# Kernel optimization log

Hardware: AMD Instinct MI355X
Metric: run time of the kernel (lower is better)

## Reference

```python
import jax, jax.numpy as jnp
import numpy as np

N, M, E = 50000, 10000, 600000
IN, H, OUT = 128, 128, 64
SLOPE = 0.01      # nn.LeakyReLU default
ATT_SLOPE = 0.2   # GAT-style attention slope
EPS = 1e-5


def _act(v):
    return jax.nn.leaky_relu(v, SLOPE)


def _graph_norm(x, w, b, a):
    # PyG GraphNorm over the node/hyperedge dim (single graph)
    mu = jnp.mean(x, axis=0, keepdims=True)
    xc = x - a * mu
    var = jnp.mean(xc * xc, axis=0, keepdims=True)
    return w * xc * jax.lax.rsqrt(var + EPS) + b


def setup_inputs() -> dict:
    key = jax.random.key(0)
    ks = iter(jax.random.split(key, 40))
    def nrm(shape):
        return jax.random.normal(next(ks), shape, jnp.float32)
    def wgt(shape):
        return nrm(shape) / np.float32(np.sqrt(shape[0]))
    return dict(
        x=nrm((N, IN)), x_struct=nrm((N, IN)), x_e=nrm((M, IN)),
        node_idx=jax.random.randint(next(ks), (E,), 0, N, dtype=jnp.int32),
        hedge_idx=jax.random.randint(next(ks), (E,), 0, M, dtype=jnp.int32),
        her_W1=wgt((IN, H)), her_b1=jnp.zeros((H,), jnp.float32),
        her_W2=wgt((H, H)), her_b2=jnp.zeros((H,), jnp.float32),
        sr_W1=wgt((IN, H)), sr_b1=jnp.zeros((H,), jnp.float32),
        sr_W2=wgt((H, H)), sr_b2=jnp.zeros((H,), jnp.float32),
        att_Wq=wgt((H, H)), att_Wk=wgt((H, H)), att_Wv=wgt((H, H)),
        ef_W=wgt((2 * H, H)), ef_b=jnp.zeros((H,), jnp.float32),
        gn1_w=jnp.ones((2 * H,), jnp.float32), gn1_b=jnp.zeros((2 * H,), jnp.float32), gn1_a=jnp.ones((2 * H,), jnp.float32),
        gn2_w=jnp.ones((H,), jnp.float32), gn2_b=jnp.zeros((H,), jnp.float32), gn2_a=jnp.ones((H,), jnp.float32),
        cls_W1=wgt((H, H)), cls_b1=jnp.zeros((H,), jnp.float32),
        cls_W2=wgt((H, OUT)), cls_b2=jnp.zeros((OUT,), jnp.float32),
    )


def _forward(x, x_struct, x_e,
             her_W1, her_b1, her_W2, her_b2,
             sr_W1, sr_b1, sr_W2, sr_b2,
             att_Wq, att_Wk, att_Wv,
             ef_W, ef_b,
             gn1_w, gn1_b, gn1_a, gn2_w, gn2_b, gn2_a,
             cls_W1, cls_b1, cls_W2, cls_b2,
             node_idx, hedge_idx):
    # --- SemanticHyperedgeRefiner: MLP [M, IN] -> [M, H]
    xe = _act(x_e @ her_W1 + her_b1) @ her_W2 + her_b2

    # --- SemanticFeatureRefiner: MLP + one node->hyperedge->node mean MP round
    h = _act(x @ sr_W1 + sr_b1)                                               # [N, H]
    ones = jnp.ones((E,), h.dtype)
    cnt_e_raw = jax.ops.segment_sum(ones, hedge_idx, M)                        # edges per hyperedge
    cnt_v_raw = jax.ops.segment_sum(ones, node_idx, N)                         # edges per node
    cnt_e = jnp.maximum(cnt_e_raw, 1.0)
    cnt_v = jnp.maximum(cnt_v_raw, 1.0)
    m_e = jax.ops.segment_sum(h[node_idx], hedge_idx, M) / cnt_e[:, None]      # [M, H]
    m_v = jax.ops.segment_sum(m_e[hedge_idx], node_idx, N) / cnt_v[:, None]    # [N, H]
    h = _act((h + m_v) @ sr_W2 + sr_b2)                                        # [N, H]

    # --- NodeHyperedgeAttention: GAT-style segment softmax per node over incident hyperedges
    q, k, v = h @ att_Wq, xe @ att_Wk, xe @ att_Wv
    s = jax.nn.leaky_relu(jnp.sum(q[node_idx] * k[hedge_idx], axis=1) / np.float32(np.sqrt(H)), ATT_SLOPE)  # [E]
    smax = jax.ops.segment_max(s, node_idx, N)
    e = jnp.exp(s - smax[node_idx])
    denom = jnp.maximum(jax.ops.segment_sum(e, node_idx, N), 1e-16)
    alpha = e / denom[node_idx]
    h = jax.ops.segment_sum(alpha[:, None] * v[hedge_idx], node_idx, N)        # [N, H]

    # --- MinAggregation: scatter-min node features into hyperedges
    agg = jax.ops.segment_min(h[node_idx], hedge_idx, M)                       # [M, H]
    agg = jnp.where((cnt_e_raw > 0.5)[:, None], agg, 0.0)                      # zero empty segments

    # --- edge_fusion: GraphNorm -> Linear(2H,H) -> LeakyReLU -> GraphNorm, then outer activation
    z = jnp.concatenate([agg, xe], axis=1)                                     # [M, 2H]
    z = _graph_norm(z, gn1_w, gn1_b, gn1_a)
    z = _act(z @ ef_W + ef_b)
    z = _graph_norm(z, gn2_w, gn2_b, gn2_a)
    z = _act(z)

    # --- Classifier (dropout inactive in eval)
    z = _act(z @ cls_W1 + cls_b1)
    return z @ cls_W2 + cls_b2                                                 # [M, OUT]


def reference(x, x_struct, x_e, node_idx, hedge_idx,
              her_W1, her_b1, her_W2, her_b2,
              sr_W1, sr_b1, sr_W2, sr_b2,
              att_Wq, att_Wk, att_Wv,
              ef_W, ef_b,
              gn1_w, gn1_b, gn1_a, gn2_w, gn2_b, gn2_a,
              cls_W1, cls_b1, cls_W2, cls_b2):
    return _forward(x, x_struct, x_e,
                    her_W1, her_b1, her_W2, her_b2,
                    sr_W1, sr_b1, sr_W2, sr_b2,
                    att_Wq, att_Wk, att_Wv,
                    ef_W, ef_b,
                    gn1_w, gn1_b, gn1_a, gn2_w, gn2_b, gn2_a,
                    cls_W1, cls_b1, cls_W2, cls_b2,
                    node_idx, hedge_idx)
```

## Files before the change

### kernel.cpp

```cpp
#include <hip/hip_runtime.h>
#include <float.h>
#include <math.h>

#define HF 128
#define SCAN_CHUNK 4096
#define NB_CSR 128
#define VPACK 12500
#define VRANGE (2 * VPACK)
#define CS_GRID 256

static inline int idiv(int a, int b) { return (a + b - 1) / b; }

__device__ inline unsigned short f2bf(float x) {
  unsigned u = __float_as_uint(x);
  return (unsigned short)((u + 0x7fffu + ((u >> 16) & 1u)) >> 16);
}
__device__ inline unsigned packbf(float a, float b) {
  return (unsigned)f2bf(a) | ((unsigned)f2bf(b) << 16);
}
#define BFLO(w) __uint_as_float((w) << 16)
#define BFHI(w) __uint_as_float((w) & 0xffff0000u)


__global__ __launch_bounds__(512) void csr_hist(const int* __restrict__ nidx,
                                                const int* __restrict__ hidx,
                                                int E, int M,
                                                int* __restrict__ HE,
                                                int* __restrict__ HV) {
  __shared__ int bins[VPACK];
  int b = blockIdx.x, y = blockIdx.y, tid = threadIdx.x;
  int chunk = (E + NB_CSR - 1) / NB_CSR;
  int e0 = b * chunk;
  int e1 = e0 + chunk; if (e1 > E) e1 = E;
  if (y == 0) {
    for (int s = tid; s < M; s += 512) bins[s] = 0;
    __syncthreads();
    for (int e = e0 + tid; e < e1; e += 512) atomicAdd(&bins[hidx[e]], 1);
    __syncthreads();
    for (int s = tid; s < M; s += 512) HE[(size_t)b * M + s] = bins[s];
  } else {
    int R = (y - 1) * VRANGE;
    int* HVr = HV + ((size_t)(y - 1) * NB_CSR + b) * VPACK;
    for (int q = tid; q < VPACK; q += 512) bins[q] = 0;
    __syncthreads();
    for (int e = e0 + tid; e < e1; e += 512) {
      int v = nidx[e] - R;
      if ((unsigned)v < (unsigned)VRANGE) atomicAdd(&bins[v >> 1], (v & 1) ? 0x10000 : 1);
    }
    __syncthreads();
    for (int q = tid; q < VPACK; q += 512) HVr[q] = bins[q];
  }
}

__global__ __launch_bounds__(256) void csr_colscan(int* __restrict__ HE,
                                                   int* __restrict__ HV,
                                                   int M, int N, int NVR,
                                                   int* __restrict__ cnt_e,
                                                   int* __restrict__ cnt_v) {
  int col = blockIdx.x * 256 + threadIdx.x;
  if (col < M) {
    int run = 0;
    for (int b = 0; b < NB_CSR; ++b) {
      size_t i = (size_t)b * M + col;
      int t = HE[i]; HE[i] = run; run += t;
    }
    cnt_e[col] = run;
  } else if (col < M + NVR * VPACK) {
    int c = col - M;
    int r = c / VPACK, q = c - r * VPACK;
    int* HVr = HV + (size_t)r * NB_CSR * VPACK;
    int run = 0;
    for (int b = 0; b < NB_CSR; ++b) {
      size_t i = (size_t)b * VPACK + q;
      int t = HVr[i]; HVr[i] = run; run += t;
    }
    int node = r * VRANGE + 2 * q;
    if (node < N) cnt_v[node] = run & 0xffff;
    if (node + 1 < N) cnt_v[node + 1] = run >> 16;
  }
}

__global__ __launch_bounds__(512) void csr_scatter(const int* __restrict__ nidx,
                                                   const int* __restrict__ hidx,
                                                   int E, int M,
                                                   const int* __restrict__ HE,
                                                   const int* __restrict__ HV,
                                                   const int* __restrict__ off_e,
                                                   const int* __restrict__ off_v,
                                                   unsigned short* __restrict__ by_h,
                                                   unsigned short* __restrict__ by_v) {
  __shared__ int bins[VPACK];
  int b = blockIdx.x, y = blockIdx.y, tid = threadIdx.x;
  int chunk = (E + NB_CSR - 1) / NB_CSR;
  int e0 = b * chunk;
  int e1 = e0 + chunk; if (e1 > E) e1 = E;
  if (y == 0) {
    for (int s = tid; s < M; s += 512) bins[s] = off_e[s] + HE[(size_t)b * M + s];
    __syncthreads();
    for (int e = e0 + tid; e < e1; e += 512) {
      int pos = atomicAdd(&bins[hidx[e]], 1);
      by_h[pos] = (unsigned short)nidx[e];
    }
  } else {
    int R = (y - 1) * VRANGE;
    const int* HVr = HV + ((size_t)(y - 1) * NB_CSR + b) * VPACK;
    for (int q = tid; q < VPACK; q += 512) bins[q] = HVr[q];
    __syncthreads();
    for (int e = e0 + tid; e < e1; e += 512) {
      int v = nidx[e];
      int vr = v - R;
      if ((unsigned)vr < (unsigned)VRANGE) {
        int old = atomicAdd(&bins[vr >> 1], (vr & 1) ? 0x10000 : 1);
        int rank = (vr & 1) ? (old >> 16) : (old & 0xffff);
        by_v[off_v[v] + rank] = (unsigned short)hidx[e];
      }
    }
  }
}


__global__ __launch_bounds__(256) void scanA2(const int* __restrict__ inE, int nE, int nbE,
                                              int* __restrict__ partE,
                                              const int* __restrict__ inV, int nV,
                                              int* __restrict__ partV) {
  const int* in; int n, b; int* partials;
  if ((int)blockIdx.x < nbE) { in = inE; n = nE; b = blockIdx.x; partials = partE; }
  else { in = inV; n = nV; b = blockIdx.x - nbE; partials = partV; }
  __shared__ int lds[256];
  int tid = threadIdx.x;
  int base = b * SCAN_CHUNK + tid * 16;
  int s = 0;
#pragma unroll
  for (int i = 0; i < 16; ++i) {
    int idx = base + i;
    if (idx < n) s += in[idx];
  }
  lds[tid] = s;
  __syncthreads();
  for (int off = 128; off; off >>= 1) {
    if (tid < off) lds[tid] += lds[tid + off];
    __syncthreads();
  }
  if (tid == 0) partials[b] = lds[0];
}

__global__ __launch_bounds__(256) void scanB2(int* __restrict__ partE, int nbE,
                                              int* __restrict__ partV, int nbV) {
  int* partials = (blockIdx.x == 0) ? partE : partV;
  int nb = (blockIdx.x == 0) ? nbE : nbV;
  __shared__ int lds[256];
  int tid = threadIdx.x;
  int v = (tid < nb) ? partials[tid] : 0;
  lds[tid] = v;
  __syncthreads();
  for (int off = 1; off < 256; off <<= 1) {
    int add = (tid >= off) ? lds[tid - off] : 0;
    __syncthreads();
    lds[tid] += add;
    __syncthreads();
  }
  if (tid < nb) partials[tid] = lds[tid] - v;
  if (tid == nb - 1) partials[nb] = lds[tid];
}

__global__ __launch_bounds__(256) void scanC2(const int* __restrict__ inE, int nE, int nbE,
                                              const int* __restrict__ partE, int* __restrict__ outE,
                                              const int* __restrict__ inV, int nV, int nbV,
                                              const int* __restrict__ partV, int* __restrict__ outV) {
  const int* in; const int* partials; int* out; int n, b, nb;
  if ((int)blockIdx.x < nbE) { in = inE; n = nE; b = blockIdx.x; partials = partE; out = outE; nb = nbE; }
  else { in = inV; n = nV; b = blockIdx.x - nbE; partials = partV; out = outV; nb = nbV; }
  __shared__ int lds[256];
  int tid = threadIdx.x;
  int base = b * SCAN_CHUNK + tid * 16;
  int vals[16];
  int s = 0;
#pragma unroll
  for (int i = 0; i < 16; ++i) {
    int idx = base + i;
    int v = (idx < n) ? in[idx] : 0;
    vals[i] = s;
    s += v;
  }
  lds[tid] = s;
  __syncthreads();
  int own = s;
  for (int off = 1; off < 256; off <<= 1) {
    int add = (tid >= off) ? lds[tid - off] : 0;
    __syncthreads();
    lds[tid] += add;
    __syncthreads();
  }
  int excl = lds[tid] - own + partials[b];
#pragma unroll
  for (int i = 0; i < 16; ++i) {
    int idx = base + i;
    if (idx < n) out[idx] = excl + vals[i];
  }
  if (b == 0 && tid == 0) out[n] = partials[nb];
}

__global__ void prep_att(const float* __restrict__ Wq, const float* __restrict__ Wv,
                         float* __restrict__ wqt, float* __restrict__ wcat) {
  int i = blockIdx.x * blockDim.x + threadIdx.x;
  if (i >= 128 * 128) return;
  int r = i >> 7, c = i & 127;
  wqt[c * 128 + r] = Wq[i] * 0.08838834764831845f;
  wcat[r * 256 + 128 + c] = Wv[i];
}


__global__ __launch_bounds__(256) void gemm64(const float* __restrict__ A,
                                              const float* __restrict__ W,
                                              const float* __restrict__ bias,
                                              float* __restrict__ out,
                                              int R, int K, int C, int act,
                                              const float* __restrict__ insc,
                                              const float* __restrict__ insh, int inact,
                                              int ldo, int obf16,
                                              unsigned short* __restrict__ out16) {
  __shared__ __align__(16) float As[64][20];
  __shared__ __align__(16) float Bs[16][64];
  int tid = threadIdx.x;
  int tx = tid & 15;
  int ty = tid >> 4;
  int rowBase = blockIdx.x * 64;
  int colBase = blockIdx.y * 64;

  float acc[4][4] = {};

  for (int k0 = 0; k0 < K; k0 += 16) {
    {
      int arow = tid >> 2, ac = (tid & 3) * 4;
      int gr = rowBase + arow;
      float4 av = make_float4(0.f, 0.f, 0.f, 0.f);
      if (gr < R) av = *(const float4*)(A + (size_t)gr * K + k0 + ac);
      if (insc) {
        float vv[4] = {av.x, av.y, av.z, av.w};
#pragma unroll
        for (int i = 0; i < 4; ++i) {
          float s = insc[k0 + ac + i], sh = insh[k0 + ac + i];
          float v = vv[i] * s + sh;
          if (inact) v = v > 0.f ? v : 0.01f * v;
          vv[i] = v;
        }
        av = make_float4(vv[0], vv[1], vv[2], vv[3]);
      }
      *(float4*)&As[arow][ac] = av;
    }
    {
      int bk = tid >> 4, bc = (tid & 15) * 4;
      *(float4*)&Bs[bk][bc] = *(const float4*)(W + (size_t)(k0 + bk) * C + colBase + bc);
    }
    __syncthreads();
#pragma unroll
    for (int kg = 0; kg < 16; kg += 4) {
      float af[4][4], bf[4][4];
#pragma unroll
      for (int i = 0; i < 4; ++i)
        *(float4*)af[i] = *(const float4*)&As[ty * 4 + i][kg];
#pragma unroll
      for (int kk = 0; kk < 4; ++kk)
        *(float4*)bf[kk] = *(const float4*)&Bs[kg + kk][tx * 4];
#pragma unroll
      for (int kk = 0; kk < 4; ++kk)
#pragma unroll
        for (int i = 0; i < 4; ++i)
#pragma unroll
          for (int j = 0; j < 4; ++j)
            acc[i][j] = fmaf(af[i][kk], bf[kk][j], acc[i][j]);
    }
    __syncthreads();
  }

#pragma unroll
  for (int i = 0; i < 4; ++i) {
    int r = rowBase + ty * 4 + i;
    if (r >= R) continue;
    float vals[4];
#pragma unroll
    for (int j = 0; j < 4; ++j) {
      float v = acc[i][j];
      if (bias) v += bias[colBase + tx * 4 + j];
      if (act) v = v > 0.f ? v : 0.01f * v;
      vals[j] = v;
    }
    if (obf16) {
      unsigned short* o16 = (unsigned short*)out;
      ushort4 w = make_ushort4(f2bf(vals[0]), f2bf(vals[1]), f2bf(vals[2]), f2bf(vals[3]));
      *(ushort4*)(o16 + (size_t)r * ldo + colBase + tx * 4) = w;
    } else {
      *(float4*)(out + (size_t)r * ldo + colBase + tx * 4) =
          make_float4(vals[0], vals[1], vals[2], vals[3]);
      if (out16) {
        uint2 w = make_uint2(packbf(vals[0], vals[1]), packbf(vals[2], vals[3]));
        *(uint2*)(out16 + (size_t)r * ldo + colBase + tx * 4) = w;
      }
    }
  }
}


__global__ __launch_bounds__(256) void seg_mean_e(const unsigned short* __restrict__ h16,
                                                  const int* __restrict__ off_e,
                                                  const unsigned short* __restrict__ by_h,
                                                  unsigned short* __restrict__ m_e16, int M) {
  int m = (blockIdx.x * blockDim.x + threadIdx.x) >> 6;
  if (m >= M) return;
  int lane = threadIdx.x & 63;
  int g = lane >> 4;
  int fl = lane & 15;
  int s = off_e[m], e1 = off_e[m + 1];
  float4 a0 = make_float4(0.f, 0.f, 0.f, 0.f), a1 = a0;
  uint4 z4 = make_uint4(0, 0, 0, 0);
  int j = s + g;
  int iC = (j + 8 < e1) ? by_h[j + 8] : 0;
  uint4 hwA = z4, hwB = z4;
  if (j < e1) {
    int i0 = by_h[j];
    hwA = *(const uint4*)(h16 + (size_t)i0 * HF + fl * 8);
  }
  if (j + 4 < e1) {
    int i1 = by_h[j + 4];
    hwB = *(const uint4*)(h16 + (size_t)i1 * HF + fl * 8);
  }
  while (j < e1) {
    uint4 hwC = z4;
    if (j + 8 < e1) hwC = *(const uint4*)(h16 + (size_t)iC * HF + fl * 8);
    int iD = (j + 12 < e1) ? by_h[j + 12] : 0;
    a0.x += BFLO(hwA.x); a0.y += BFHI(hwA.x); a0.z += BFLO(hwA.y); a0.w += BFHI(hwA.y);
    a1.x += BFLO(hwA.z); a1.y += BFHI(hwA.z); a1.z += BFLO(hwA.w); a1.w += BFHI(hwA.w);
    hwA = hwB; hwB = hwC; iC = iD;
    j += 4;
  }
#pragma unroll
  for (int mask = 16; mask <= 32; mask <<= 1) {
    a0.x += __shfl_xor(a0.x, mask); a0.y += __shfl_xor(a0.y, mask);
    a0.z += __shfl_xor(a0.z, mask); a0.w += __shfl_xor(a0.w, mask);
    a1.x += __shfl_xor(a1.x, mask); a1.y += __shfl_xor(a1.y, mask);
    a1.z += __shfl_xor(a1.z, mask); a1.w += __shfl_xor(a1.w, mask);
  }
  if (g == 0) {
    int cnt = e1 - s;
    float r = 1.f / (float)(cnt > 0 ? cnt : 1);
    uint4 w = make_uint4(packbf(a0.x * r, a0.y * r), packbf(a0.z * r, a0.w * r),
                         packbf(a1.x * r, a1.y * r), packbf(a1.z * r, a1.w * r));
    *(uint4*)(m_e16 + (size_t)m * HF + fl * 8) = w;
  }
}

__global__ __launch_bounds__(256) void seg_mean_v_add(float* __restrict__ h,
                                                      const unsigned short* __restrict__ m_e16,
                                                      const int* __restrict__ off_v,
                                                      const unsigned short* __restrict__ by_v,
                                                      int N) {
  int n = (blockIdx.x * blockDim.x + threadIdx.x) >> 6;
  if (n >= N) return;
  int lane = threadIdx.x & 63;
  int g = lane >> 4;
  int fl = lane & 15;
  int s = off_v[n], e1 = off_v[n + 1];
  float4 a0 = make_float4(0.f, 0.f, 0.f, 0.f), a1 = a0;
  uint4 z4 = make_uint4(0, 0, 0, 0);
  int j = s + g;
  int iC = (j + 8 < e1) ? by_v[j + 8] : 0;
  uint4 hwA = z4, hwB = z4;
  if (j < e1) {
    int i0 = by_v[j];
    hwA = *(const uint4*)(m_e16 + (size_t)i0 * HF + fl * 8);
  }
  if (j + 4 < e1) {
    int i1 = by_v[j + 4];
    hwB = *(const uint4*)(m_e16 + (size_t)i1 * HF + fl * 8);
  }
  while (j < e1) {
    uint4 hwC = z4;
    if (j + 8 < e1) hwC = *(const uint4*)(m_e16 + (size_t)iC * HF + fl * 8);
    int iD = (j + 12 < e1) ? by_v[j + 12] : 0;
    a0.x += BFLO(hwA.x); a0.y += BFHI(hwA.x); a0.z += BFLO(hwA.y); a0.w += BFHI(hwA.y);
    a1.x += BFLO(hwA.z); a1.y += BFHI(hwA.z); a1.z += BFLO(hwA.w); a1.w += BFHI(hwA.w);
    hwA = hwB; hwB = hwC; iC = iD;
    j += 4;
  }
#pragma unroll
  for (int mask = 16; mask <= 32; mask <<= 1) {
    a0.x += __shfl_xor(a0.x, mask); a0.y += __shfl_xor(a0.y, mask);
    a0.z += __shfl_xor(a0.z, mask); a0.w += __shfl_xor(a0.w, mask);
    a1.x += __shfl_xor(a1.x, mask); a1.y += __shfl_xor(a1.y, mask);
    a1.z += __shfl_xor(a1.z, mask); a1.w += __shfl_xor(a1.w, mask);
  }
  if (g == 0) {
    int cnt = e1 - s;
    float r = 1.f / (float)(cnt > 0 ? cnt : 1);
    float* hp = h + (size_t)n * HF + fl * 8;
    float4 h0 = *(const float4*)hp;
    float4 h1 = *(const float4*)(hp + 4);
    *(float4*)hp = make_float4(h0.x + a0.x * r, h0.y + a0.y * r, h0.z + a0.z * r, h0.w + a0.w * r);
    *(float4*)(hp + 4) = make_float4(h1.x + a1.x * r, h1.y + a1.y * r, h1.z + a1.z * r, h1.w + a1.w * r);
  }
}

__global__ __launch_bounds__(256) void att_fused(const float* __restrict__ q,
                                                 const unsigned short* __restrict__ kv,
                                                 const int* __restrict__ off_v,
                                                 const unsigned short* __restrict__ by_v,
                                                 unsigned short* __restrict__ ho16, int N) {
  int n = (blockIdx.x * blockDim.x + threadIdx.x) >> 6;
  if (n >= N) return;
  int lane = threadIdx.x & 63;
  int g = lane >> 4;
  int fl = lane & 15;
  int s0 = off_v[n], s1 = off_v[n + 1];
  const float* qp = q + (size_t)n * HF + fl * 8;
  float4 q0 = *(const float4*)qp;
  float4 q1 = *(const float4*)(qp + 4);
  float m = -INFINITY, l = 0.f;
  float4 a0 = make_float4(0.f, 0.f, 0.f, 0.f), a1 = a0;
  uint4 z4 = make_uint4(0, 0, 0, 0);
  int j = s0 + g;
  int iC = (j + 8 < s1) ? by_v[j + 8] : 0;
  uint4 kwA = z4, vwA = z4, kwB = z4, vwB = z4;
  if (j < s1) {
    const unsigned short* b = kv + (size_t)by_v[j] * 256 + fl * 8;
    kwA = *(const uint4*)b;
    vwA = *(const uint4*)(b + 128);
  }
  if (j + 4 < s1) {
    const unsigned short* b = kv + (size_t)by_v[j + 4] * 256 + fl * 8;
    kwB = *(const uint4*)b;
    vwB = *(const uint4*)(b + 128);
  }
  while (j < s1) {
    uint4 kwC = z4, vwC = z4;
    if (j + 8 < s1) {
      const unsigned short* b = kv + (size_t)iC * 256 + fl * 8;
      kwC = *(const uint4*)b;
      vwC = *(const uint4*)(b + 128);
    }
    int iD = (j + 12 < s1) ? by_v[j + 12] : 0;
    float d = q0.x * BFLO(kwA.x) + q0.y * BFHI(kwA.x) + q0.z * BFLO(kwA.y) + q0.w * BFHI(kwA.y)
            + q1.x * BFLO(kwA.z) + q1.y * BFHI(kwA.z) + q1.z * BFLO(kwA.w) + q1.w * BFHI(kwA.w);
    d += __shfl_xor(d, 1);
    d += __shfl_xor(d, 2);
    d += __shfl_xor(d, 4);
    d += __shfl_xor(d, 8);
    d = d > 0.f ? d : 0.2f * d;
    if (d > m + 8.f) {
      float sc = __expf(m - d);
      l *= sc;
      a0.x *= sc; a0.y *= sc; a0.z *= sc; a0.w *= sc;
      a1.x *= sc; a1.y *= sc; a1.z *= sc; a1.w *= sc;
      m = d;
    }
    float p = __expf(d - m);
    l += p;
    a0.x += p * BFLO(vwA.x); a0.y += p * BFHI(vwA.x);
    a0.z += p * BFLO(vwA.y); a0.w += p * BFHI(vwA.y);
    a1.x += p * BFLO(vwA.z); a1.y += p * BFHI(vwA.z);
    a1.z += p * BFLO(vwA.w); a1.w += p * BFHI(vwA.w);
    kwA = kwB; vwA = vwB; kwB = kwC; vwB = vwC; iC = iD;
    j += 4;
  }
#pragma unroll
  for (int mask = 16; mask <= 32; mask <<= 1) {
    float m2 = __shfl_xor(m, mask);
    float l2 = __shfl_xor(l, mask);
    float b0x = __shfl_xor(a0.x, mask), b0y = __shfl_xor(a0.y, mask);
    float b0z = __shfl_xor(a0.z, mask), b0w = __shfl_xor(a0.w, mask);
    float b1x = __shfl_xor(a1.x, mask), b1y = __shfl_xor(a1.y, mask);
    float b1z = __shfl_xor(a1.z, mask), b1w = __shfl_xor(a1.w, mask);
    float mn = fmaxf(fmaxf(m, m2), -1e30f);
    float ea = __expf(m - mn), eb = __expf(m2 - mn);
    l = l * ea + l2 * eb;
    a0.x = a0.x * ea + b0x * eb; a0.y = a0.y * ea + b0y * eb;
    a0.z = a0.z * ea + b0z * eb; a0.w = a0.w * ea + b0w * eb;
    a1.x = a1.x * ea + b1x * eb; a1.y = a1.y * ea + b1y * eb;
    a1.z = a1.z * ea + b1z * eb; a1.w = a1.w * ea + b1w * eb;
    m = fmaxf(m, m2);
  }
  if (g == 0) {
    float inv = 1.f / fmaxf(l, 1e-16f);
    uint4 w = make_uint4(packbf(a0.x * inv, a0.y * inv), packbf(a0.z * inv, a0.w * inv),
                         packbf(a1.x * inv, a1.y * inv), packbf(a1.z * inv, a1.w * inv));
    *(uint4*)(ho16 + (size_t)n * HF + fl * 8) = w;
  }
}

__global__ __launch_bounds__(256) void seg_min_z(const unsigned short* __restrict__ ho16,
                                                 const int* __restrict__ off_e,
                                                 const unsigned short* __restrict__ by_h,
                                                 const float* __restrict__ xe,
                                                 float* __restrict__ z, int M) {
  int m = (blockIdx.x * blockDim.x + threadIdx.x) >> 6;
  if (m >= M) return;
  int lane = threadIdx.x & 63;
  int g = lane >> 4;
  int fl = lane & 15;
  int s = off_e[m], e1 = off_e[m + 1];
  float4 a0 = make_float4(FLT_MAX, FLT_MAX, FLT_MAX, FLT_MAX), a1 = a0;
  uint4 z4 = make_uint4(0, 0, 0, 0);
  int j = s + g;
  int iC = (j + 8 < e1) ? by_h[j + 8] : 0;
  uint4 hwA = z4, hwB = z4;
  if (j < e1) {
    int i0 = by_h[j];
    hwA = *(const uint4*)(ho16 + (size_t)i0 * HF + fl * 8);
  }
  if (j + 4 < e1) {
    int i1 = by_h[j + 4];
    hwB = *(const uint4*)(ho16 + (size_t)i1 * HF + fl * 8);
  }
  while (j < e1) {
    uint4 hwC = z4;
    if (j + 8 < e1) hwC = *(const uint4*)(ho16 + (size_t)iC * HF + fl * 8);
    int iD = (j + 12 < e1) ? by_h[j + 12] : 0;
    a0.x = fminf(a0.x, BFLO(hwA.x)); a0.y = fminf(a0.y, BFHI(hwA.x));
    a0.z = fminf(a0.z, BFLO(hwA.y)); a0.w = fminf(a0.w, BFHI(hwA.y));
    a1.x = fminf(a1.x, BFLO(hwA.z)); a1.y = fminf(a1.y, BFHI(hwA.z));
    a1.z = fminf(a1.z, BFLO(hwA.w)); a1.w = fminf(a1.w, BFHI(hwA.w));
    hwA = hwB; hwB = hwC; iC = iD;
    j += 4;
  }
#pragma unroll
  for (int mask = 16; mask <= 32; mask <<= 1) {
    a0.x = fminf(a0.x, __shfl_xor(a0.x, mask)); a0.y = fminf(a0.y, __shfl_xor(a0.y, mask));
    a0.z = fminf(a0.z, __shfl_xor(a0.z, mask)); a0.w = fminf(a0.w, __shfl_xor(a0.w, mask));
    a1.x = fminf(a1.x, __shfl_xor(a1.x, mask)); a1.y = fminf(a1.y, __shfl_xor(a1.y, mask));
    a1.z = fminf(a1.z, __shfl_xor(a1.z, mask)); a1.w = fminf(a1.w, __shfl_xor(a1.w, mask));
  }
  if (g == 0) {
    bool nz = (e1 > s);
    float* op = z + (size_t)m * 256 + fl * 8;
    *(float4*)op = nz ? a0 : make_float4(0.f, 0.f, 0.f, 0.f);
    *(float4*)(op + 4) = nz ? a1 : make_float4(0.f, 0.f, 0.f, 0.f);
  } else if (g == 1) {
    const float* xp = xe + (size_t)m * HF + fl * 8;
    float* op = z + (size_t)m * 256 + 128 + fl * 8;
    *(float4*)op = *(const float4*)xp;
    *(float4*)(op + 4) = *(const float4*)(xp + 4);
  }
}


__global__ __launch_bounds__(1024) void colstats_part(const float* __restrict__ z, int rows, int C,
                                                      float* __restrict__ part) {
  int tid = threadIdx.x;
  int RL = 1024 / C;
  int col = tid & (C - 1);
  int ro = tid / C;
  float s1 = 0.f, s2 = 0.f;
  for (int r = blockIdx.x * RL + ro; r < rows; r += gridDim.x * RL) {
    float v = z[(size_t)r * C + col];
    s1 += v;
    s2 += v * v;
  }
  __shared__ float l1[1024], l2[1024];
  l1[tid] = s1;
  l2[tid] = s2;
  __syncthreads();
  for (int off = 512; off >= C; off >>= 1) {
    if (tid < off) { l1[tid] += l1[tid + off]; l2[tid] += l2[tid + off]; }
    __syncthreads();
  }
  if (tid < C) {
    part[(size_t)blockIdx.x * 2 * C + tid] = l1[tid];
    part[(size_t)blockIdx.x * 2 * C + C + tid] = l2[tid];
  }
}

__global__ void colstats_fin(const float* __restrict__ part, int nb, int C,
                             const float* __restrict__ w, const float* __restrict__ b,
                             const float* __restrict__ a, float invrows,
                             float* __restrict__ sc, float* __restrict__ sh) {
  int col = threadIdx.x;
  if (col >= C) return;
  float s1 = 0.f, s2 = 0.f;
#pragma unroll 8
  for (int i = 0; i < nb; ++i) {
    s1 += part[(size_t)i * 2 * C + col];
    s2 += part[(size_t)i * 2 * C + C + col];
  }
  float mu = s1 * invrows;
  float ex2 = s2 * invrows;
  float av = a[col];
  float var = ex2 - 2.f * av * mu * mu + av * av * mu * mu;
  float s = w[col] * rsqrtf(var + 1e-5f);
  sc[col] = s;
  sh[col] = b[col] - av * mu * s;
}


extern "C" void kernel_launch(void* const* d_in, const int* in_sizes, int n_in,
                              void* d_out, int out_size, void* d_ws, size_t ws_size,
                              hipStream_t stream) {
  const float* x        = (const float*)d_in[0];
  const float* x_e      = (const float*)d_in[2];
  const int*   node_idx = (const int*)d_in[3];
  const int*   hedge_idx= (const int*)d_in[4];
  const float* her_W1   = (const float*)d_in[5];
  const float* her_b1   = (const float*)d_in[6];
  const float* her_W2   = (const float*)d_in[7];
  const float* her_b2   = (const float*)d_in[8];
  const float* sr_W1    = (const float*)d_in[9];
  const float* sr_b1    = (const float*)d_in[10];
  const float* sr_W2    = (const float*)d_in[11];
  const float* sr_b2    = (const float*)d_in[12];
  const float* att_Wq   = (const float*)d_in[13];
  const float* att_Wk   = (const float*)d_in[14];
  const float* att_Wv   = (const float*)d_in[15];
  const float* ef_W     = (const float*)d_in[16];
  const float* ef_b     = (const float*)d_in[17];
  const float* gn1_w    = (const float*)d_in[18];
  const float* gn1_b    = (const float*)d_in[19];
  const float* gn1_a    = (const float*)d_in[20];
  const float* gn2_w    = (const float*)d_in[21];
  const float* gn2_b    = (const float*)d_in[22];
  const float* gn2_a    = (const float*)d_in[23];
  const float* cls_W1   = (const float*)d_in[24];
  const float* cls_b1   = (const float*)d_in[25];
  const float* cls_W2   = (const float*)d_in[26];
  const float* cls_b2   = (const float*)d_in[27];

  const int N = in_sizes[0] / HF;
  const int M = in_sizes[2] / HF;
  const int E = in_sizes[3];
  const int NVR = idiv(N, VRANGE);

  char* wp = (char*)d_ws;
  float* part1 = (float*)wp; wp += (size_t)CS_GRID * 512 * 4;
  float* part2 = (float*)wp; wp += (size_t)CS_GRID * 256 * 4;
  int* cnt_e = (int*)wp; wp += (size_t)M * 4;
  int* cnt_v = (int*)wp; wp += (size_t)N * 4;
  int* off_e = (int*)wp; wp += (size_t)(M + 1) * 4;
  int* off_v = (int*)wp; wp += (size_t)(N + 1) * 4;
  unsigned short* by_h = (unsigned short*)wp; wp += ((size_t)E * 2 + 3) & ~(size_t)3;
  unsigned short* by_v = (unsigned short*)wp; wp += ((size_t)E * 2 + 3) & ~(size_t)3;
  int* part_e = (int*)wp; wp += 257 * 4;
  int* part_v = (int*)wp; wp += 257 * 4;
  float* sc1 = (float*)wp; wp += 256 * 4;
  float* sh1 = (float*)wp; wp += 256 * 4;
  float* sc2 = (float*)wp; wp += 128 * 4;
  float* sh2 = (float*)wp; wp += 128 * 4;
  wp = (char*)(((uintptr_t)wp + 255) & ~(uintptr_t)255);
  float* wqt  = (float*)wp; wp += (size_t)128 * 128 * 4;
  float* wcat = (float*)wp; wp += (size_t)128 * 256 * 4;
  float* h   = (float*)wp; wp += (size_t)N * HF * 4;
  float* h2  = (float*)wp; wp += (size_t)N * HF * 4;
  float* xe  = (float*)wp; wp += (size_t)M * HF * 4;
  float* kvf = (float*)wp; wp += (size_t)M * 256 * 4;
  float* z2  = (float*)wp; wp += (size_t)M * HF * 4;
  unsigned short* h16   = (unsigned short*)wp; wp += (size_t)N * HF * 2;
  unsigned short* ho16  = (unsigned short*)wp; wp += (size_t)N * HF * 2;
  unsigned short* m_e16 = (unsigned short*)wp; wp += (size_t)M * HF * 2;

  unsigned short* kv = (unsigned short*)kvf;
  float* t1  = kvf;
  float* z   = h2;
  float* c1  = h;

  int* HE = (int*)h;
  int* HV = HE + (size_t)NB_CSR * M;

  csr_hist<<<dim3(NB_CSR, 1 + NVR), 512, 0, stream>>>(node_idx, hedge_idx, E, M, HE, HV);
  csr_colscan<<<idiv(M + NVR * VPACK, 256), 256, 0, stream>>>(HE, HV, M, N, NVR, cnt_e, cnt_v);
  int nbE = idiv(M, SCAN_CHUNK);
  int nbV = idiv(N, SCAN_CHUNK);
  scanA2<<<nbE + nbV, 256, 0, stream>>>(cnt_e, M, nbE, part_e, cnt_v, N, part_v);
  scanB2<<<2, 256, 0, stream>>>(part_e, nbE, part_v, nbV);
  scanC2<<<nbE + nbV, 256, 0, stream>>>(cnt_e, M, nbE, part_e, off_e, cnt_v, N, nbV, part_v, off_v);
  csr_scatter<<<dim3(NB_CSR, 1 + NVR), 512, 0, stream>>>(node_idx, hedge_idx, E, M, HE, HV,
                                                         off_e, off_v, by_h, by_v);

  prep_att<<<64, 256, 0, stream>>>(att_Wq, att_Wv, wqt, wcat);
  gemm64<<<dim3(2, 2), 256, 0, stream>>>(att_Wk, wqt, nullptr, wcat, 128, 128, 128, 0,
                                         nullptr, nullptr, 0, 256, 0, nullptr);

  dim3 blk(256);
  gemm64<<<dim3(idiv(M, 64), 2), blk, 0, stream>>>(x_e, her_W1, her_b1, t1, M, HF, HF, 1,
                                                   nullptr, nullptr, 0, HF, 0, nullptr);
  gemm64<<<dim3(idiv(M, 64), 2), blk, 0, stream>>>(t1, her_W2, her_b2, xe, M, HF, HF, 0,
                                                   nullptr, nullptr, 0, HF, 0, nullptr);
  gemm64<<<dim3(idiv(N, 64), 2), blk, 0, stream>>>(x, sr_W1, sr_b1, h, N, HF, HF, 1,
                                                   nullptr, nullptr, 0, HF, 0, h16);
  seg_mean_e<<<idiv(M * 64, 256), blk, 0, stream>>>(h16, off_e, by_h, m_e16, M);
  seg_mean_v_add<<<idiv(N * 64, 256), blk, 0, stream>>>(h, m_e16, off_v, by_v, N);
  gemm64<<<dim3(idiv(N, 64), 2), blk, 0, stream>>>(h, sr_W2, sr_b2, h2, N, HF, HF, 1,
                                                   nullptr, nullptr, 0, HF, 0, nullptr);
  gemm64<<<dim3(idiv(M, 64), 4), blk, 0, stream>>>(xe, wcat, nullptr, (float*)kv, M, HF, 256, 0,
                                                   nullptr, nullptr, 0, 256, 1, nullptr);
  att_fused<<<idiv(N * 64, 256), blk, 0, stream>>>(h2, kv, off_v, by_v, ho16, N);
  seg_min_z<<<idiv(M * 64, 256), blk, 0, stream>>>(ho16, off_e, by_h, xe, z, M);
  colstats_part<<<CS_GRID, 1024, 0, stream>>>(z, M, 256, part1);
  colstats_fin<<<1, 256, 0, stream>>>(part1, CS_GRID, 256, gn1_w, gn1_b, gn1_a,
                                      1.f / (float)M, sc1, sh1);
  gemm64<<<dim3(idiv(M, 64), 2), blk, 0, stream>>>(z, ef_W, ef_b, z2, M, 2 * HF, HF, 1,
                                                   sc1, sh1, 0, HF, 0, nullptr);
  colstats_part<<<CS_GRID, 1024, 0, stream>>>(z2, M, 128, part2);
  colstats_fin<<<1, 128, 0, stream>>>(part2, CS_GRID, 128, gn2_w, gn2_b, gn2_a,
                                      1.f / (float)M, sc2, sh2);
  gemm64<<<dim3(idiv(M, 64), 2), blk, 0, stream>>>(z2, cls_W1, cls_b1, c1, M, HF, HF, 1,
                                                   sc2, sh2, 1, HF, 0, nullptr);
  gemm64<<<dim3(idiv(M, 64), 1), blk, 0, stream>>>(c1, cls_W2, cls_b2, (float*)d_out, M, HF, 64, 0,
                                                   nullptr, nullptr, 0, 64, 0, nullptr);
}
```

Before: 385.5 us.

## Batch independent GEMMs and segment-mean into shared multi-launch kernels

Independent GEMMs (sr_W1, her_W1, Wk·Wq fold; sr_W2 with the kv projection) are merged into single launches that dispatch by block index, and the her_W2 GEMM is co-launched with the hyperedge segment mean. This cuts launch count and lets small M-sized GEMMs fill the GPU alongside larger work. Separately, the attention gather loop's prefetch depth drops from two steps ahead to one, lowering register use at the cost of less latency hiding. Dispatching by block index adds some branching and register pressure from the merged kernel bodies.

```diff
diff --git a/kernel.cpp b/kernel.cpp
--- a/kernel.cpp
+++ b/kernel.cpp
@@ -210,22 +210,23 @@
 }
 
 
-__global__ __launch_bounds__(256) void gemm64(const float* __restrict__ A,
-                                              const float* __restrict__ W,
-                                              const float* __restrict__ bias,
-                                              float* __restrict__ out,
-                                              int R, int K, int C, int act,
-                                              const float* __restrict__ insc,
-                                              const float* __restrict__ insh, int inact,
-                                              int ldo, int obf16,
-                                              unsigned short* __restrict__ out16) {
+__device__ __forceinline__ void gemm64_body(const float* __restrict__ A,
+                                            const float* __restrict__ W,
+                                            const float* __restrict__ bias,
+                                            float* __restrict__ out,
+                                            int R, int K, int C, int act,
+                                            const float* __restrict__ insc,
+                                            const float* __restrict__ insh, int inact,
+                                            int ldo, int obf16,
+                                            unsigned short* __restrict__ out16,
+                                            int bx, int by) {
   __shared__ __align__(16) float As[64][20];
   __shared__ __align__(16) float Bs[16][64];
   int tid = threadIdx.x;
   int tx = tid & 15;
   int ty = tid >> 4;
-  int rowBase = blockIdx.x * 64;
-  int colBase = blockIdx.y * 64;
+  int rowBase = bx * 64;
+  int colBase = by * 64;
 
   float acc[4][4] = {};
 
@@ -300,12 +301,37 @@
   }
 }
 
-
-__global__ __launch_bounds__(256) void seg_mean_e(const unsigned short* __restrict__ h16,
-                                                  const int* __restrict__ off_e,
-                                                  const unsigned short* __restrict__ by_h,
-                                                  unsigned short* __restrict__ m_e16, int M) {
-  int m = (blockIdx.x * blockDim.x + threadIdx.x) >> 6;
+struct GArgs {
+  const float* A; const float* W; const float* bias; float* out;
+  int R, K, C, act;
+  const float* insc; const float* insh; int inact, ldo, obf16;
+  unsigned short* out16;
+  int nbx, nb;
+};
+
+__global__ __launch_bounds__(256) void gemm64(GArgs g) {
+  gemm64_body(g.A, g.W, g.bias, g.out, g.R, g.K, g.C, g.act, g.insc, g.insh, g.inact,
+              g.ldo, g.obf16, g.out16, blockIdx.x % g.nbx, blockIdx.x / g.nbx);
+}
+
+__global__ __launch_bounds__(256) void gemm64_multi(GArgs g0, GArgs g1, GArgs g2) {
+  int b = blockIdx.x;
+  GArgs g = g0;
+  if (b >= g0.nb) {
+    b -= g0.nb;
+    if (b < g1.nb) g = g1;
+    else { b -= g1.nb; g = g2; }
+  }
+  gemm64_body(g.A, g.W, g.bias, g.out, g.R, g.K, g.C, g.act, g.insc, g.insh, g.inact,
+              g.ldo, g.obf16, g.out16, b % g.nbx, b / g.nbx);
+}
+
+
+__device__ __forceinline__ void seg_mean_e_body(const unsigned short* __restrict__ h16,
+                                                const int* __restrict__ off_e,
+                                                const unsigned short* __restrict__ by_h,
+                                                unsigned short* __restrict__ m_e16, int M, int bx) {
+  int m = (bx * 256 + (int)threadIdx.x) >> 6;
   if (m >= M) return;
   int lane = threadIdx.x & 63;
   int g = lane >> 4;
@@ -347,6 +373,20 @@
                          packbf(a1.x * r, a1.y * r), packbf(a1.z * r, a1.w * r));
     *(uint4*)(m_e16 + (size_t)m * HF + fl * 8) = w;
   }
+}
+
+__global__ __launch_bounds__(256) void gemm_segmean(GArgs g,
+                                                    const unsigned short* __restrict__ h16,
+                                                    const int* __restrict__ off_e,
+                                                    const unsigned short* __restrict__ by_h,
+                                                    unsigned short* __restrict__ m_e16, int M) {
+  int b = blockIdx.x;
+  if (b < g.nb) {
+    gemm64_body(g.A, g.W, g.bias, g.out, g.R, g.K, g.C, g.act, g.insc, g.insh, g.inact,
+                g.ldo, g.obf16, g.out16, b % g.nbx, b / g.nbx);
+    return;
+  }
+  seg_mean_e_body(h16, off_e, by_h, m_e16, M, b - g.nb);
 }
 
 __global__ __launch_bounds__(256) void seg_mean_v_add(float* __restrict__ h,
@@ -416,30 +456,23 @@
   float4 q1 = *(const float4*)(qp + 4);
   float m = -INFINITY, l = 0.f;
   float4 a0 = make_float4(0.f, 0.f, 0.f, 0.f), a1 = a0;
-  uint4 z4 = make_uint4(0, 0, 0, 0);
   int j = s0 + g;
-  int iC = (j + 8 < s1) ? by_v[j + 8] : 0;
-  uint4 kwA = z4, vwA = z4, kwB = z4, vwB = z4;
+  uint4 kw = make_uint4(0, 0, 0, 0), vw = kw;
   if (j < s1) {
-    const unsigned short* b = kv + (size_t)by_v[j] * 256 + fl * 8;
-    kwA = *(const uint4*)b;
-    vwA = *(const uint4*)(b + 128);
-  }
-  if (j + 4 < s1) {
-    const unsigned short* b = kv + (size_t)by_v[j + 4] * 256 + fl * 8;
-    kwB = *(const uint4*)b;
-    vwB = *(const uint4*)(b + 128);
+    const unsigned short* base = kv + (size_t)by_v[j] * 256 + fl * 8;
+    kw = *(const uint4*)base;
+    vw = *(const uint4*)(base + 128);
   }
   while (j < s1) {
-    uint4 kwC = z4, vwC = z4;
-    if (j + 8 < s1) {
-      const unsigned short* b = kv + (size_t)iC * 256 + fl * 8;
-      kwC = *(const uint4*)b;
-      vwC = *(const uint4*)(b + 128);
-    }
-    int iD = (j + 12 < s1) ? by_v[j + 12] : 0;
-    float d = q0.x * BFLO(kwA.x) + q0.y * BFHI(kwA.x) + q0.z * BFLO(kwA.y) + q0.w * BFHI(kwA.y)
-            + q1.x * BFLO(kwA.z) + q1.y * BFHI(kwA.z) + q1.z * BFLO(kwA.w) + q1.w * BFHI(kwA.w);
+    int jn = j + 4;
+    uint4 kw2 = make_uint4(0, 0, 0, 0), vw2 = kw2;
+    if (jn < s1) {
+      const unsigned short* b2 = kv + (size_t)by_v[jn] * 256 + fl * 8;
+      kw2 = *(const uint4*)b2;
+      vw2 = *(const uint4*)(b2 + 128);
+    }
+    float d = q0.x * BFLO(kw.x) + q0.y * BFHI(kw.x) + q0.z * BFLO(kw.y) + q0.w * BFHI(kw.y)
+            + q1.x * BFLO(kw.z) + q1.y * BFHI(kw.z) + q1.z * BFLO(kw.w) + q1.w * BFHI(kw.w);
     d += __shfl_xor(d, 1);
     d += __shfl_xor(d, 2);
     d += __shfl_xor(d, 4);
@@ -454,12 +487,11 @@
     }
     float p = __expf(d - m);
     l += p;
-    a0.x += p * BFLO(vwA.x); a0.y += p * BFHI(vwA.x);
-    a0.z += p * BFLO(vwA.y); a0.w += p * BFHI(vwA.y);
-    a1.x += p * BFLO(vwA.z); a1.y += p * BFHI(vwA.z);
-    a1.z += p * BFLO(vwA.w); a1.w += p * BFHI(vwA.w);
-    kwA = kwB; vwA = vwB; kwB = kwC; vwB = vwC; iC = iD;
-    j += 4;
+    a0.x += p * BFLO(vw.x); a0.y += p * BFHI(vw.x);
+    a0.z += p * BFLO(vw.y); a0.w += p * BFHI(vw.y);
+    a1.x += p * BFLO(vw.z); a1.y += p * BFHI(vw.z);
+    a1.z += p * BFLO(vw.w); a1.w += p * BFHI(vw.w);
+    kw = kw2; vw = vw2; j = jn;
   }
 #pragma unroll
   for (int mask = 16; mask <= 32; mask <<= 1) {
@@ -672,34 +704,36 @@
                                                          off_e, off_v, by_h, by_v);
 
   prep_att<<<64, 256, 0, stream>>>(att_Wq, att_Wv, wqt, wcat);
-  gemm64<<<dim3(2, 2), 256, 0, stream>>>(att_Wk, wqt, nullptr, wcat, 128, 128, 128, 0,
-                                         nullptr, nullptr, 0, 256, 0, nullptr);
 
   dim3 blk(256);
-  gemm64<<<dim3(idiv(M, 64), 2), blk, 0, stream>>>(x_e, her_W1, her_b1, t1, M, HF, HF, 1,
-                                                   nullptr, nullptr, 0, HF, 0, nullptr);
-  gemm64<<<dim3(idiv(M, 64), 2), blk, 0, stream>>>(t1, her_W2, her_b2, xe, M, HF, HF, 0,
-                                                   nullptr, nullptr, 0, HF, 0, nullptr);
-  gemm64<<<dim3(idiv(N, 64), 2), blk, 0, stream>>>(x, sr_W1, sr_b1, h, N, HF, HF, 1,
-                                                   nullptr, nullptr, 0, HF, 0, h16);
-  seg_mean_e<<<idiv(M * 64, 256), blk, 0, stream>>>(h16, off_e, by_h, m_e16, M);
+  int nbxN = idiv(N, 64), nbxM = idiv(M, 64);
+
+  GArgs gsr1 = {x, sr_W1, sr_b1, h, N, HF, HF, 1, nullptr, nullptr, 0, HF, 0, h16, nbxN, nbxN * 2};
+  GArgs gher1 = {x_e, her_W1, her_b1, t1, M, HF, HF, 1, nullptr, nullptr, 0, HF, 0, nullptr, nbxM, nbxM * 2};
+  GArgs gwk = {att_Wk, wqt, nullptr, wcat, 128, 128, 128, 0, nullptr, nullptr, 0, 256, 0, nullptr, 2, 4};
+  gemm64_multi<<<gsr1.nb + gher1.nb + gwk.nb, blk, 0, stream>>>(gsr1, gher1, gwk);
+
+  GArgs gher2 = {t1, her_W2, her_b2, xe, M, HF, HF, 0, nullptr, nullptr, 0, HF, 0, nullptr, nbxM, nbxM * 2};
+  gemm_segmean<<<gher2.nb + idiv(M * 64, 256), blk, 0, stream>>>(gher2, h16, off_e, by_h, m_e16, M);
+
   seg_mean_v_add<<<idiv(N * 64, 256), blk, 0, stream>>>(h, m_e16, off_v, by_v, N);
-  gemm64<<<dim3(idiv(N, 64), 2), blk, 0, stream>>>(h, sr_W2, sr_b2, h2, N, HF, HF, 1,
-                                                   nullptr, nullptr, 0, HF, 0, nullptr);
-  gemm64<<<dim3(idiv(M, 64), 4), blk, 0, stream>>>(xe, wcat, nullptr, (float*)kv, M, HF, 256, 0,
-                                                   nullptr, nullptr, 0, 256, 1, nullptr);
+
+  GArgs gsr2 = {h, sr_W2, sr_b2, h2, N, HF, HF, 1, nullptr, nullptr, 0, HF, 0, nullptr, nbxN, nbxN * 2};
+  GArgs gkv = {xe, wcat, nullptr, (float*)kv, M, HF, 256, 0, nullptr, nullptr, 0, 256, 1, nullptr, nbxM, nbxM * 4};
+  gemm64_multi<<<gsr2.nb + gkv.nb, blk, 0, stream>>>(gsr2, gkv, gkv);
+
   att_fused<<<idiv(N * 64, 256), blk, 0, stream>>>(h2, kv, off_v, by_v, ho16, N);
   seg_min_z<<<idiv(M * 64, 256), blk, 0, stream>>>(ho16, off_e, by_h, xe, z, M);
   colstats_part<<<CS_GRID, 1024, 0, stream>>>(z, M, 256, part1);
   colstats_fin<<<1, 256, 0, stream>>>(part1, CS_GRID, 256, gn1_w, gn1_b, gn1_a,
                                       1.f / (float)M, sc1, sh1);
-  gemm64<<<dim3(idiv(M, 64), 2), blk, 0, stream>>>(z, ef_W, ef_b, z2, M, 2 * HF, HF, 1,
-                                                   sc1, sh1, 0, HF, 0, nullptr);
+  GArgs gef = {z, ef_W, ef_b, z2, M, 2 * HF, HF, 1, sc1, sh1, 0, HF, 0, nullptr, nbxM, nbxM * 2};
+  gemm64<<<gef.nb, blk, 0, stream>>>(gef);
   colstats_part<<<CS_GRID, 1024, 0, stream>>>(z2, M, 128, part2);
   colstats_fin<<<1, 128, 0, stream>>>(part2, CS_GRID, 128, gn2_w, gn2_b, gn2_a,
                                       1.f / (float)M, sc2, sh2);
-  gemm64<<<dim3(idiv(M, 64), 2), blk, 0, stream>>>(z2, cls_W1, cls_b1, c1, M, HF, HF, 1,
-                                                   sc2, sh2, 1, HF, 0, nullptr);
-  gemm64<<<dim3(idiv(M, 64), 1), blk, 0, stream>>>(c1, cls_W2, cls_b2, (float*)d_out, M, HF, 64, 0,
-                                                   nullptr, nullptr, 0, 64, 0, nullptr);
-}
+  GArgs gc1 = {z2, cls_W1, cls_b1, c1, M, HF, HF, 1, sc2, sh2, 1, HF, 0, nullptr, nbxM, nbxM * 2};
+  gemm64<<<gc1.nb, blk, 0, stream>>>(gc1);
+  GArgs gc2 = {c1, cls_W2, cls_b2, (float*)d_out, M, HF, 64, 0, nullptr, nullptr, 0, 64, 0, nullptr, nbxM, nbxM};
+  gemm64<<<gc2.nb, blk, 0, stream>>>(gc2);
+}
```

Result: faster. 344.3 us, median of 2 (-10.7%).
